# Kernel tuning notes

Hardware: AMD Instinct MI355X
Metric: run time of the kernel (lower is better)

The kernel has to match this reference:

```python
import jax, jax.numpy as jnp
import numpy as np

N = 4096
D = 256
TAU = 0.8
LAM = 0.5
K0, K1 = 64, 128


def setup_inputs() -> dict:
    key = jax.random.key(0)
    ks = jax.random.split(key, 20)
    s = 1.0 / np.sqrt(D)
    pos = (jax.random.uniform(ks[3], (N, N)) < 0.01).astype(jnp.float32)
    pos = pos.at[jnp.arange(N), jnp.arange(N)].set(1.0)  # guarantee a positive per row
    return {
        'z_mp': jax.random.normal(ks[0], (N, D), jnp.float32),
        'z_sc': jax.random.normal(ks[1], (N, D), jnp.float32),
        'feat': jax.random.normal(ks[2], (N, D), jnp.float32),
        'pos': pos,
        'im2c0': jax.random.randint(ks[4], (N,), 0, K0, jnp.int32),
        'im2c1': jax.random.randint(ks[5], (N,), 0, K1, jnp.int32),
        'centroids0': jax.random.normal(ks[6], (K0, D), jnp.float32),
        'centroids1': jax.random.normal(ks[7], (K1, D), jnp.float32),
        'density0': jax.random.uniform(ks[8], (K0,), jnp.float32) + 0.5,
        'density1': jax.random.uniform(ks[9], (K1,), jnp.float32) + 0.5,
        'pW1': jax.random.normal(ks[10], (D, D), jnp.float32) * s * 1.414,
        'pb1': jnp.zeros((D,), jnp.float32),
        'pW2': jax.random.normal(ks[11], (D, D), jnp.float32) * s * 1.414,
        'pb2': jnp.zeros((D,), jnp.float32),
        'mW1': jax.random.normal(ks[12], (D, D), jnp.float32) * s,
        'mb1': jnp.zeros((D,), jnp.float32),
        'mW2': jax.random.normal(ks[13], (D, D), jnp.float32) * s,
        'mb2': jnp.zeros((D,), jnp.float32),
    }


def _mlp(x, W1, b1, W2, b2):
    # nn.Linear -> ELU -> nn.Linear (torch Linear: x @ W.T + b)
    return jax.nn.elu(x @ W1.T + b1) @ W2.T + b2


def _sim(z1, z2, tau):
    n1 = jnp.linalg.norm(z1, axis=-1, keepdims=True)
    n2 = jnp.linalg.norm(z2, axis=-1, keepdims=True)
    return jnp.exp((z1 @ z2.T) / (n1 @ n2.T) / tau)


def _nce(sim_matrix, pos):
    m = sim_matrix / (sim_matrix.sum(axis=1, keepdims=True) + 1e-8)
    return -jnp.log((m * pos).sum(axis=-1)).mean()


def _pocl(z_anchor, z, im2cs, centroids, densities):
    n = z_anchor.shape[0]
    # weight[a,b] = #levels where a,b share a cluster (original: coo @ coo.T summed)
    sames = [(c[:, None] == c[None, :]).astype(z.dtype) for c in im2cs]
    weight = sames[0] + sames[1]
    node_prototypes = jnp.zeros_like(z)
    loss = jnp.float32(0.0)
    for same, im2c, protos, dens in zip(sames, im2cs, centroids, densities):
        # original aliases weight_clus = weight, so masking accumulates in-place
        weight = weight * same
        c = (weight @ z) / weight.sum(axis=1)[:, None]
        node_prototypes = node_prototypes + 0.1 * c
        phi = dens[im2c]
        pos_p = jnp.exp((z_anchor * node_prototypes).sum(axis=1) / phi)
        neg_p = jnp.exp((z_anchor @ protos.T) / dens).mean(axis=1) * n
        loss = loss + (-jnp.log(pos_p / neg_p)).mean()
    return loss / len(im2cs)


def reference(z_mp, z_sc, feat, pos, im2c0, im2c1, centroids0, centroids1,
              density0, density1, pW1, pb1, pW2, pb2, mW1, mb1, mW2, mb2):
    z_proj_mp = _mlp(z_mp, pW1, pb1, pW2, pb2)
    z_proj_sc = _mlp(z_sc, pW1, pb1, pW2, pb2)
    m_mp2sc = _sim(z_proj_mp, z_proj_sc, TAU)
    lori_mp = _nce(m_mp2sc, pos)
    lori_sc = _nce(m_mp2sc.T, pos)
    proto_loss = _pocl(z_sc, z_mp, [im2c0, im2c1],
                       [centroids0, centroids1], [density0, density1])
    mp_intra = _mlp(z_mp, mW1, mb1, mW2, mb2)
    loss_intramp = _nce(_sim(mp_intra, mp_intra, 0.05), pos)
    proj_mp_feat = _mlp(z_mp, pW1, pb1, pW2, pb2)
    proj_feat = _mlp(feat, pW1, pb1, pW2, pb2)
    lori_mpfeat = _nce(_sim(proj_mp_feat, proj_feat, TAU), pos)
    lori_featmp = _nce(_sim(proj_feat, proj_mp_feat, TAU), pos)
    return (LAM * lori_mp + (1 - LAM) * lori_sc + 0.3 * loss_intramp
            + proto_loss + 0.01 * lori_mpfeat + 0.01 * lori_featmp)
```

## Files before the change

kernel.cpp:

```cpp
#include <hip/hip_runtime.h>
#include <math.h>


#define NROWS 4096
#define DIM   256
#define ND    ((size_t)NROWS * DIM)

typedef unsigned short u16;
typedef unsigned int   u32;
typedef unsigned long long u64;
typedef __attribute__((ext_vector_type(8))) short bf16x8;
typedef __attribute__((ext_vector_type(4))) float f32x4;

__device__ __forceinline__ u16 f2bf(float f) {
    u32 u = __float_as_uint(f);
    return (u16)((u + 0x7fffu + ((u >> 16) & 1u)) >> 16);
}
__device__ __forceinline__ float bf2f(u16 h) {
    return __uint_as_float(((u32)h) << 16);
}

__device__ __forceinline__ void gload16(const u16* g, u16* l) {
    __builtin_amdgcn_global_load_lds(
        (const __attribute__((address_space(1))) u32*)g,
        (__attribute__((address_space(3))) u32*)l, 16, 0, 0);
}

template<int ROWS>
__device__ __forceinline__ void stage_panel(const u16* P, int kk, u16* S, int tid) {
#pragma unroll
    for (int p = 0; p < ROWS / 64; ++p) {
        const int ch = p * 256 + tid, row = ch >> 2, seg = ch & 3;
        gload16(P + (size_t)row * DIM + kk + seg * 8, &S[ch * 8]);
    }
}

__device__ __forceinline__ void wait_lgkm0() {
    asm volatile("s_waitcnt lgkmcnt(0)" ::: "memory");
    __builtin_amdgcn_sched_barrier(0);
}
template<int N> __device__ __forceinline__ void wait_vm() {
    if constexpr (N == 0)      asm volatile("s_waitcnt vmcnt(0)" ::: "memory");
    else if constexpr (N == 3) asm volatile("s_waitcnt vmcnt(3)" ::: "memory");
    else if constexpr (N == 4) asm volatile("s_waitcnt vmcnt(4)" ::: "memory");
    else if constexpr (N == 6) asm volatile("s_waitcnt vmcnt(6)" ::: "memory");
}

struct Ptr3 { const float* s0; const float* s1; const float* s2; };
__global__ __launch_bounds__(256) void cvt_in(Ptr3 p, u16* __restrict__ dst)
{
    const int z = blockIdx.y;
    const float* s = z == 0 ? p.s0 : (z == 1 ? p.s1 : p.s2);
    u16* d = dst + (size_t)z * ND;
    const int i = blockIdx.x * 256 + threadIdx.x;
    const float4 v = ((const float4*)s)[i];
    ushort4 o;
    o.x = f2bf(v.x); o.y = f2bf(v.y); o.z = f2bf(v.z); o.w = f2bf(v.w);
    ((ushort4*)d)[i] = o;
}
struct Ptr4 { const float* s0; const float* s1; const float* s2; const float* s3; };
__global__ __launch_bounds__(256) void cvt_w(Ptr4 p, u16* __restrict__ dst)
{
    const int z = blockIdx.y;
    const float* s = z == 0 ? p.s0 : (z == 1 ? p.s1 : (z == 2 ? p.s2 : p.s3));
    u16* d = dst + (size_t)z * 65536;
    const int i = blockIdx.x * 256 + threadIdx.x;
    const float4 v = ((const float4*)s)[i];
    ushort4 o;
    o.x = f2bf(v.x); o.y = f2bf(v.y); o.z = f2bf(v.z); o.w = f2bf(v.w);
    ((ushort4*)d)[i] = o;
}
__global__ __launch_bounds__(256) void cvt_cent(const float* __restrict__ c0,
                                                const float* __restrict__ c1,
                                                u16* __restrict__ CB)
{
    const int i = blockIdx.x * 256 + threadIdx.x;
    const float4 v = (i < 4096) ? ((const float4*)c0)[i]
                                : ((const float4*)c1)[i - 4096];
    ushort4 o;
    o.x = f2bf(v.x); o.y = f2bf(v.y); o.z = f2bf(v.z); o.w = f2bf(v.w);
    ((ushort4*)CB)[i] = o;
}

__global__ __launch_bounds__(256) void posbits(const float* __restrict__ pos,
                                               u64* __restrict__ bits)
{
    const int i = blockIdx.x;
    const int w = threadIdx.x >> 6, l = threadIdx.x & 63;
#pragma unroll
    for (int c = 0; c < 16; ++c) {
        const int j = c * 256 + w * 64 + l;
        const float v = pos[(size_t)i * NROWS + j];
        const u64 m = __ballot(v != 0.f);
        if (l == 0) bits[(size_t)i * 64 + c * 4 + w] = m;
    }
}

template<int ACT, int REMAP>
__global__ __launch_bounds__(256, 4) void mlp_mfma(const u16* __restrict__ IN,
                                                   const u16* __restrict__ Wp,
                                                   const u16* __restrict__ Wm,
                                                   const float* __restrict__ bp,
                                                   const float* __restrict__ bm,
                                                   u16* __restrict__ OUT)
{
    __shared__ __align__(16) u16 As[3][64 * 32];
    __shared__ __align__(16) u16 Bs[3][128 * 32];
    const int tid = threadIdx.x;
    const int bx = blockIdx.x, by = blockIdx.y;
    const bool intra = by >= 192;
    const int arow = (REMAP && intra) ? (by - 192) * 64 : by * 64;
    const u16* A = IN + (size_t)arow * DIM;
    const u16* B = (intra ? Wm : Wp) + (size_t)(bx * 128) * DIM;
    const float* bias = intra ? bm : bp;
    const int l = tid & 63, w = tid >> 6, wr = w >> 1, wc = w & 1;
    const int lr = l & 15, lk = l >> 4;

    f32x4 acc[2][4] = {};
    stage_panel<64>(A, 0, As[0], tid);
    stage_panel<128>(B, 0, Bs[0], tid);
    stage_panel<64>(A, 32, As[1], tid);
    stage_panel<128>(B, 32, Bs[1], tid);
    wait_vm<3>();
    __builtin_amdgcn_s_barrier();
#pragma unroll
    for (int t = 0; t < 8; ++t) {
        bf16x8 a[2], b[4];
#pragma unroll
        for (int mi = 0; mi < 2; ++mi)
            a[mi] = *(const bf16x8*)&As[t % 3][(wr * 32 + mi * 16 + lr) * 32 + lk * 8];
#pragma unroll
        for (int ni = 0; ni < 4; ++ni)
            b[ni] = *(const bf16x8*)&Bs[t % 3][(wc * 64 + ni * 16 + lr) * 32 + lk * 8];
        if (t < 6) {
            stage_panel<64>(A, (t + 2) * 32, As[(t + 2) % 3], tid);
            stage_panel<128>(B, (t + 2) * 32, Bs[(t + 2) % 3], tid);
        }
        wait_lgkm0();
#pragma unroll
        for (int mi = 0; mi < 2; ++mi)
#pragma unroll
            for (int ni = 0; ni < 4; ++ni)
                acc[mi][ni] = __builtin_amdgcn_mfma_f32_16x16x32_bf16(a[mi], b[ni], acc[mi][ni], 0, 0, 0);
        if (t < 6)      { wait_vm<3>(); __builtin_amdgcn_s_barrier(); }
        else if (t < 7) { wait_vm<0>(); __builtin_amdgcn_s_barrier(); }
    }

    const int j0 = bx * 128;
    float bv[4];
#pragma unroll
    for (int ni = 0; ni < 4; ++ni) bv[ni] = bias[j0 + wc * 64 + ni * 16 + lr];
#pragma unroll
    for (int mi = 0; mi < 2; ++mi)
#pragma unroll
        for (int r = 0; r < 4; ++r) {
            const int row = by * 64 + wr * 32 + mi * 16 + lk * 4 + r;
#pragma unroll
            for (int ni = 0; ni < 4; ++ni) {
                float v = acc[mi][ni][r] + bv[ni];
                if (ACT) v = v > 0.f ? v : expm1f(v);
                OUT[(size_t)row * DIM + j0 + wc * 64 + ni * 16 + lr] = f2bf(v);
            }
        }
}

__global__ __launch_bounds__(256) void rownorm_bf(u16* __restrict__ X)
{
    const int w = threadIdx.x >> 6, l = threadIdx.x & 63;
    const int row = blockIdx.x * 4 + w;
    ushort4* p = (ushort4*)(X + (size_t)row * DIM) + l;
    ushort4 u = *p;
    const float a = bf2f(u.x), b = bf2f(u.y), c = bf2f(u.z), d = bf2f(u.w);
    float ss = a * a + b * b + c * c + d * d;
#pragma unroll
    for (int m = 1; m < 64; m <<= 1) ss += __shfl_xor(ss, m);
    const float inv = rsqrtf(ss);
    u.x = f2bf(a * inv); u.y = f2bf(b * inv); u.z = f2bf(c * inv); u.w = f2bf(d * inv);
    *p = u;
}

__global__ __launch_bounds__(256, 3) void simstat3c(const u16* __restrict__ PROJ,
                                                    const u64* __restrict__ bits,
                                                    float* __restrict__ ST)
{
    const int bid = blockIdx.x;
    int z, by, bx;
    if (bid < 1024) {
        z = 0;
        const int x = bid & 7, j = bid >> 3;
        by = (x >> 1) * 8 + (j >> 4);
        bx = (x & 1) * 16 + (j & 15);
    } else if (bid < 1552) {
        z = 1;
        const int u = bid - 1024;
        const int t = (u & 7) * 66 + (u >> 3);
        int r = (int)((65.0f - sqrtf(4225.0f - 8.0f * (float)t)) * 0.5f);
        int off = 32 * r - (r * (r - 1)) / 2;
        if (t < off)                   { --r; off -= 33 - r; }
        else if (t >= off + (32 - r))  { off += 32 - r; ++r; }
        by = r; bx = r + (t - off);
    } else {
        z = 2;
        const int v = bid - 1552;
        const int x = v & 7, j = v >> 3;
        by = (x >> 1) * 8 + (j >> 4);
        bx = (x & 1) * 16 + (j & 15);
    }

    __shared__ __align__(16) u16 As[3][128 * 32];
    __shared__ __align__(16) u16 Bs[3][128 * 32];
    const int tid = threadIdx.x;
    int ao, bo;
    float* rsr; float* rsc;
    switch (z) {
        case 0:  ao = 0; bo = 1; rsr = ST + 0;     rsc = ST + 8192;  break;
        case 1:  ao = 3; bo = 3; rsr = ST + 16384; rsc = ST + 16384; break;
        default: ao = 0; bo = 2; rsr = ST + 24576; rsc = ST + 32768; break;
    }
    const float invtau = (z == 1) ? 20.f : 1.25f;
    const bool docol = (z != 1) || (bx > by);
    const int i0 = by * 128, j0 = bx * 128;
    const u16* A = PROJ + (size_t)ao * ND + (size_t)i0 * DIM;
    const u16* B = PROJ + (size_t)bo * ND + (size_t)j0 * DIM;
    const int l = tid & 63, w = tid >> 6, wr = w >> 1, wc = w & 1;
    const int lr = l & 15, lk = l >> 4;

    f32x4 acc[4][4] = {};
    stage_panel<128>(A, 0, As[0], tid);
    stage_panel<128>(B, 0, Bs[0], tid);
    stage_panel<128>(A, 32, As[1], tid);
    stage_panel<128>(B, 32, Bs[1], tid);
    wait_vm<4>();
    __builtin_amdgcn_s_barrier();
#pragma unroll
    for (int t = 0; t < 8; ++t) {
        bf16x8 a[4], b[4];
#pragma unroll
        for (int mi = 0; mi < 4; ++mi)
            a[mi] = *(const bf16x8*)&As[t % 3][(wr * 64 + mi * 16 + lr) * 32 + lk * 8];
#pragma unroll
        for (int ni = 0; ni < 4; ++ni)
            b[ni] = *(const bf16x8*)&Bs[t % 3][(wc * 64 + ni * 16 + lr) * 32 + lk * 8];
        if (t < 6) {
            stage_panel<128>(A, (t + 2) * 32, As[(t + 2) % 3], tid);
            stage_panel<128>(B, (t + 2) * 32, Bs[(t + 2) % 3], tid);
        }
        wait_lgkm0();
#pragma unroll
        for (int mi = 0; mi < 4; ++mi)
#pragma unroll
            for (int ni = 0; ni < 4; ++ni)
                acc[mi][ni] = __builtin_amdgcn_mfma_f32_16x16x32_bf16(a[mi], b[ni], acc[mi][ni], 0, 0, 0);
        if (t < 6)      { wait_vm<4>(); __builtin_amdgcn_s_barrier(); }
        else if (t < 7) { wait_vm<0>(); __builtin_amdgcn_s_barrier(); }
    }

#pragma unroll
    for (int mi = 0; mi < 4; ++mi)
#pragma unroll
        for (int ni = 0; ni < 4; ++ni)
#pragma unroll
            for (int r = 0; r < 4; ++r)
                acc[mi][ni][r] = __expf(acc[mi][ni][r] * invtau);

#pragma unroll
    for (int mi = 0; mi < 4; ++mi)
#pragma unroll
        for (int r = 0; r < 4; ++r) {
            const int i = i0 + wr * 64 + mi * 16 + lk * 4 + r;
            const u64 pw = bits[(size_t)i * 64 + bx * 2 + wc];
            float rsum = 0.f, psum = 0.f;
#pragma unroll
            for (int ni = 0; ni < 4; ++ni) {
                const float ev = acc[mi][ni][r];
                rsum += ev;
                psum += ((pw >> (ni * 16 + lr)) & 1ull) ? ev : 0.f;
            }
#pragma unroll
            for (int m = 1; m < 16; m <<= 1) {
                rsum += __shfl_xor(rsum, m);
                psum += __shfl_xor(psum, m);
            }
            if (lr == 0) {
                atomicAdd(&rsr[i], rsum);
                atomicAdd(&rsr[4096 + i], psum);
            }
        }

    if (docol) {
#pragma unroll
        for (int ni = 0; ni < 4; ++ni) {
            const int j = j0 + wc * 64 + ni * 16 + lr;
            const u64 pw = bits[(size_t)j * 64 + by * 2 + wr];
            float csum = 0.f, qsum = 0.f;
#pragma unroll
            for (int mi = 0; mi < 4; ++mi)
#pragma unroll
                for (int r = 0; r < 4; ++r) {
                    const float ev = acc[mi][ni][r];
                    csum += ev;
                    qsum += ((pw >> (mi * 16 + lk * 4 + r)) & 1ull) ? ev : 0.f;
                }
            csum += __shfl_xor(csum, 16); csum += __shfl_xor(csum, 32);
            qsum += __shfl_xor(qsum, 16); qsum += __shfl_xor(qsum, 32);
            if (lk == 0) {
                atomicAdd(&rsc[j], csum);
                atomicAdd(&rsc[4096 + j], qsum);
            }
        }
    }
}

__global__ __launch_bounds__(256, 4) void gcent_mfma(const u16* __restrict__ Zb,
                                                     const u16* __restrict__ CB,
                                                     float* __restrict__ G)
{
    __shared__ __align__(16) u16 As[3][128 * 32];
    __shared__ __align__(16) u16 Bs[3][64 * 32];
    const int tid = threadIdx.x;
    const int bx = blockIdx.x, by = blockIdx.y;
    const int i0 = by * 128, j0 = bx * 64;
    const u16* A = Zb + (size_t)i0 * DIM;
    const u16* B = CB + (size_t)j0 * DIM;
    const int l = tid & 63, w = tid >> 6, wr = w >> 1, wc = w & 1;
    const int lr = l & 15, lk = l >> 4;

    f32x4 acc[4][2] = {};
    stage_panel<128>(A, 0, As[0], tid);
    stage_panel<64>(B, 0, Bs[0], tid);
    stage_panel<128>(A, 32, As[1], tid);
    stage_panel<64>(B, 32, Bs[1], tid);
    wait_vm<3>();
    __builtin_amdgcn_s_barrier();
#pragma unroll
    for (int t = 0; t < 8; ++t) {
        bf16x8 a[4], b[2];
#pragma unroll
        for (int mi = 0; mi < 4; ++mi)
            a[mi] = *(const bf16x8*)&As[t % 3][(wr * 64 + mi * 16 + lr) * 32 + lk * 8];
#pragma unroll
        for (int ni = 0; ni < 2; ++ni)
            b[ni] = *(const bf16x8*)&Bs[t % 3][(wc * 32 + ni * 16 + lr) * 32 + lk * 8];
        if (t < 6) {
            stage_panel<128>(A, (t + 2) * 32, As[(t + 2) % 3], tid);
            stage_panel<64>(B, (t + 2) * 32, Bs[(t + 2) % 3], tid);
        }
        wait_lgkm0();
#pragma unroll
        for (int mi = 0; mi < 4; ++mi)
#pragma unroll
            for (int ni = 0; ni < 2; ++ni)
                acc[mi][ni] = __builtin_amdgcn_mfma_f32_16x16x32_bf16(a[mi], b[ni], acc[mi][ni], 0, 0, 0);
        if (t < 6)      { wait_vm<3>(); __builtin_amdgcn_s_barrier(); }
        else if (t < 7) { wait_vm<0>(); __builtin_amdgcn_s_barrier(); }
    }

#pragma unroll
    for (int mi = 0; mi < 4; ++mi)
#pragma unroll
        for (int r = 0; r < 4; ++r) {
            const int row = i0 + wr * 64 + mi * 16 + lk * 4 + r;
#pragma unroll
            for (int ni = 0; ni < 2; ++ni)
                G[(size_t)row * 192 + j0 + wc * 32 + ni * 16 + lr] = acc[mi][ni][r];
        }
}

__global__ __launch_bounds__(256) void scatter_pairs(const float* __restrict__ z,
                                                     const int* __restrict__ i0a,
                                                     const int* __restrict__ i1a,
                                                     float* __restrict__ S01,
                                                     float* __restrict__ cnt01)
{
    const int b = blockIdx.x, d = threadIdx.x;
    const int p = i0a[b] * 128 + i1a[b];
    atomicAdd(&S01[(size_t)p * DIM + d], z[(size_t)b * DIM + d]);
    if (d == 0) atomicAdd(&cnt01[p], 1.f);
}

__global__ __launch_bounds__(256) void reduce_pairs(const float* __restrict__ S01,
                                                    const float* __restrict__ cnt01,
                                                    float* __restrict__ S0,
                                                    float* __restrict__ cnt0)
{
    const int k0 = blockIdx.x, d = threadIdx.x;
    float s = 0.f;
    for (int k1 = 0; k1 < 128; ++k1)
        s += S01[(size_t)(k0 * 128 + k1) * DIM + d];
    S0[(size_t)k0 * DIM + d] = s;
    __shared__ float c[128];
    if (d < 128) c[d] = cnt01[k0 * 128 + d];
    __syncthreads();
    if (d == 0) {
        float t = 0.f;
        for (int i = 0; i < 128; ++i) t += c[i];
        cnt0[k0] = t;
    }
}

__global__ __launch_bounds__(256) void pocl_row(const float* __restrict__ z_sc,
                                                const int* __restrict__ i0a,
                                                const int* __restrict__ i1a,
                                                const float* __restrict__ S0,
                                                const float* __restrict__ S01,
                                                const float* __restrict__ cnt0,
                                                const float* __restrict__ cnt01,
                                                const float* __restrict__ G,
                                                const float* __restrict__ d0,
                                                const float* __restrict__ d1,
                                                float* __restrict__ L1,
                                                float* __restrict__ L2)
{
    const int w = threadIdx.x >> 6, l = threadIdx.x & 63;
    const int a = blockIdx.x * 4 + w;
    const int k0 = i0a[a], k1 = i1a[a];
    const int p = k0 * 128 + k1;
    const float n0 = cnt0[k0], n01 = cnt01[p];
    const float inv1 = 1.f / (n0 + n01), inv2 = 1.f / n01;
    const float4 s0  = *(const float4*)&S0[(size_t)k0 * DIM + l * 4];
    const float4 s01 = *(const float4*)&S01[(size_t)p * DIM + l * 4];
    const float4 zd  = *(const float4*)&z_sc[(size_t)a * DIM + l * 4];

    float dot1 = 0.f, dot2 = 0.f;
    {
        const float c1x = (s0.x + s01.x) * inv1, c2x = s01.x * inv2;
        const float c1y = (s0.y + s01.y) * inv1, c2y = s01.y * inv2;
        const float c1z = (s0.z + s01.z) * inv1, c2z = s01.z * inv2;
        const float c1w = (s0.w + s01.w) * inv1, c2w = s01.w * inv2;
        dot1 = zd.x * c1x + zd.y * c1y + zd.z * c1z + zd.w * c1w;
        dot2 = zd.x * (c1x + c2x) + zd.y * (c1y + c2y) + zd.z * (c1z + c2z) + zd.w * (c1w + c2w);
    }
    dot1 *= 0.1f; dot2 *= 0.1f;
#pragma unroll
    for (int m = 1; m < 64; m <<= 1) {
        dot1 += __shfl_xor(dot1, m);
        dot2 += __shfl_xor(dot2, m);
    }

    const float x0 = G[(size_t)a * 192 + l] / d0[l];
    float M0 = x0;
#pragma unroll
    for (int m = 1; m < 64; m <<= 1) M0 = fmaxf(M0, __shfl_xor(M0, m));
    float e0 = __expf(x0 - M0);
#pragma unroll
    for (int m = 1; m < 64; m <<= 1) e0 += __shfl_xor(e0, m);

    const float x1a = G[(size_t)a * 192 + 64 + l] / d1[l];
    const float x1b = G[(size_t)a * 192 + 128 + l] / d1[64 + l];
    float M1 = fmaxf(x1a, x1b);
#pragma unroll
    for (int m = 1; m < 64; m <<= 1) M1 = fmaxf(M1, __shfl_xor(M1, m));
    float e1 = __expf(x1a - M1) + __expf(x1b - M1);
#pragma unroll
    for (int m = 1; m < 64; m <<= 1) e1 += __shfl_xor(e1, m);

    if (l == 0) {
        const float lneg1 = M0 + logf(e0) - logf(64.f)  + logf(4096.f);
        const float lneg2 = M1 + logf(e1) - logf(128.f) + logf(4096.f);
        L1[a] = lneg1 - dot1 / d0[k0];
        L2[a] = lneg2 - dot2 / d1[k1];
    }
}

__global__ __launch_bounds__(256) void final_reduce(const float* __restrict__ st,
                                                    const float* __restrict__ L1,
                                                    const float* __restrict__ L2,
                                                    float* __restrict__ out)
{
    const int t = threadIdx.x;
    const float* rs0 = st + 0;      const float* pr0 = st + 4096;
    const float* rs1 = st + 8192;   const float* pr1 = st + 12288;
    const float* rs2 = st + 16384;  const float* pr2 = st + 20480;
    const float* rs3 = st + 24576;  const float* pr3 = st + 28672;
    const float* rs4 = st + 32768;  const float* pr4 = st + 36864;

    float acc = 0.f;
    for (int i = t; i < NROWS; i += 256) {
        const float lmp = logf(rs0[i] + 1e-8f) - logf(pr0[i]);
        const float lsc = logf(rs1[i] + 1e-8f) - logf(pr1[i]);
        const float lin = logf(rs2[i] + 1e-8f) - logf(pr2[i]);
        const float lmf = logf(rs3[i] + 1e-8f) - logf(pr3[i]);
        const float lfm = logf(rs4[i] + 1e-8f) - logf(pr4[i]);
        acc += 0.5f * (lmp + lsc) + 0.3f * lin
             + 0.01f * (lmf + lfm) + 0.5f * (L1[i] + L2[i]);
    }
    __shared__ float red[256];
    red[t] = acc; __syncthreads();
    for (int s = 128; s > 0; s >>= 1) {
        if (t < s) red[t] += red[t + s];
        __syncthreads();
    }
    if (t == 0) out[0] = red[0] * (1.f / 4096.f);
}

extern "C" void kernel_launch(void* const* d_in, const int* in_sizes, int n_in,
                              void* d_out, int out_size, void* d_ws, size_t ws_size,
                              hipStream_t stream)
{
    const float* z_mp = (const float*)d_in[0];
    const float* z_sc = (const float*)d_in[1];
    const float* feat = (const float*)d_in[2];
    const float* pos  = (const float*)d_in[3];
    const int*   im0  = (const int*)d_in[4];
    const int*   im1  = (const int*)d_in[5];
    const float* c0   = (const float*)d_in[6];
    const float* c1   = (const float*)d_in[7];
    const float* d0   = (const float*)d_in[8];
    const float* d1   = (const float*)d_in[9];
    const float* pW1  = (const float*)d_in[10];
    const float* pb1  = (const float*)d_in[11];
    const float* pW2  = (const float*)d_in[12];
    const float* pb2  = (const float*)d_in[13];
    const float* mW1  = (const float*)d_in[14];
    const float* mb1  = (const float*)d_in[15];
    const float* mW2  = (const float*)d_in[16];
    const float* mb2  = (const float*)d_in[17];
    float* out = (float*)d_out;
    float* ws  = (float*)d_ws;
    (void)in_sizes; (void)n_in; (void)out_size; (void)ws_size;

    float* ST   = ws;
    float* S0f  = ST + 40960;
    float* CN0  = S0f + 16384;
    float* CN01 = CN0 + 64;
    float* S01f = CN01 + 8192;
    float* ZEND = S01f + (size_t)8192 * DIM;
    float* G    = ZEND;
    float* L1   = G + (size_t)NROWS * 192;
    float* L2   = L1 + NROWS;
    u64*  bits  = (u64*)(L2 + NROWS);
    u16*  INb   = (u16*)(bits + (size_t)NROWS * 64);
    u16*  Hb    = INb + 3 * ND;
    u16*  PROJ  = Hb + 4 * ND;
    u16*  Wb    = PROJ + 4 * ND;
    u16*  CB    = Wb + 4 * 65536;

    hipMemsetAsync(ws, 0, (size_t)(ZEND - ws) * sizeof(float), stream);

    const dim3 blk(256);

    Ptr3 pin{z_mp, z_sc, feat};
    cvt_in<<<dim3(1024, 3), blk, 0, stream>>>(pin, INb);
    Ptr4 pw{pW1, pW2, mW1, mW2};
    cvt_w<<<dim3(64, 4), blk, 0, stream>>>(pw, Wb);
    cvt_cent<<<48, blk, 0, stream>>>(c0, c1, CB);

    posbits<<<NROWS, blk, 0, stream>>>(pos, bits);

    mlp_mfma<1, 1><<<dim3(2, 256), blk, 0, stream>>>(INb, Wb, Wb + 2 * 65536,
                                                     pb1, mb1, Hb);
    mlp_mfma<0, 0><<<dim3(2, 256), blk, 0, stream>>>(Hb, Wb + 65536, Wb + 3 * 65536,
                                                     pb2, mb2, PROJ);
    rownorm_bf<<<4096, blk, 0, stream>>>(PROJ);

    simstat3c<<<2576, blk, 0, stream>>>(PROJ, bits, ST);

    scatter_pairs<<<NROWS, blk, 0, stream>>>(z_mp, im0, im1, S01f, CN01);
    reduce_pairs<<<64, blk, 0, stream>>>(S01f, CN01, S0f, CN0);
    gcent_mfma<<<dim3(3, 32), blk, 0, stream>>>(INb + ND, CB, G);
    pocl_row<<<1024, blk, 0, stream>>>(z_sc, im0, im1, S0f, S01f, CN0, CN01,
                                       G, d0, d1, L1, L2);

    final_reduce<<<1, blk, 0, stream>>>(ST, L1, L2, out);
}
```

Before: 163.9 us.

## Shrink GEMM tiles to double-buffered 64-wide tiles and drop symmetric-tile skipping

```diff
diff --git a/kernel.cpp b/kernel.cpp
--- a/kernel.cpp
+++ b/kernel.cpp
@@ -41,9 +41,8 @@
 }
 template<int N> __device__ __forceinline__ void wait_vm() {
     if constexpr (N == 0)      asm volatile("s_waitcnt vmcnt(0)" ::: "memory");
+    else if constexpr (N == 2) asm volatile("s_waitcnt vmcnt(2)" ::: "memory");
     else if constexpr (N == 3) asm volatile("s_waitcnt vmcnt(3)" ::: "memory");
-    else if constexpr (N == 4) asm volatile("s_waitcnt vmcnt(4)" ::: "memory");
-    else if constexpr (N == 6) asm volatile("s_waitcnt vmcnt(6)" ::: "memory");
 }
 
 struct Ptr3 { const float* s0; const float* s1; const float* s2; };
@@ -104,15 +103,107 @@
                                                    const float* __restrict__ bm,
                                                    u16* __restrict__ OUT)
 {
-    __shared__ __align__(16) u16 As[3][64 * 32];
-    __shared__ __align__(16) u16 Bs[3][128 * 32];
+    __shared__ __align__(16) u16 As[2][64 * 32];
+    __shared__ __align__(16) u16 Bs[2][64 * 32];
     const int tid = threadIdx.x;
     const int bx = blockIdx.x, by = blockIdx.y;
     const bool intra = by >= 192;
     const int arow = (REMAP && intra) ? (by - 192) * 64 : by * 64;
     const u16* A = IN + (size_t)arow * DIM;
-    const u16* B = (intra ? Wm : Wp) + (size_t)(bx * 128) * DIM;
+    const u16* B = (intra ? Wm : Wp) + (size_t)(bx * 64) * DIM;
     const float* bias = intra ? bm : bp;
+    const int l = tid & 63, w = tid >> 6, wr = w >> 1, wc = w & 1;
+    const int lr = l & 15, lk = l >> 4;
+
+    f32x4 acc[2][2] = {};
+    stage_panel<64>(A, 0, As[0], tid);
+    stage_panel<64>(B, 0, Bs[0], tid);
+    stage_panel<64>(A, 32, As[1], tid);
+    stage_panel<64>(B, 32, Bs[1], tid);
+    wait_vm<2>();
+    __builtin_amdgcn_s_barrier();
+#pragma unroll
+    for (int t = 0; t < 8; ++t) {
+        bf16x8 a[2], b[2];
+#pragma unroll
+        for (int mi = 0; mi < 2; ++mi)
+            a[mi] = *(const bf16x8*)&As[t & 1][(wr * 32 + mi * 16 + lr) * 32 + lk * 8];
+#pragma unroll
+        for (int ni = 0; ni < 2; ++ni)
+            b[ni] = *(const bf16x8*)&Bs[t & 1][(wc * 32 + ni * 16 + lr) * 32 + lk * 8];
+        wait_lgkm0();
+        __builtin_amdgcn_s_barrier();
+        if (t < 6) {
+            stage_panel<64>(A, (t + 2) * 32, As[t & 1], tid);
+            stage_panel<64>(B, (t + 2) * 32, Bs[t & 1], tid);
+        }
+#pragma unroll
+        for (int mi = 0; mi < 2; ++mi)
+#pragma unroll
+            for (int ni = 0; ni < 2; ++ni)
+                acc[mi][ni] = __builtin_amdgcn_mfma_f32_16x16x32_bf16(a[mi], b[ni], acc[mi][ni], 0, 0, 0);
+        if (t < 6)      { wait_vm<2>(); __builtin_amdgcn_s_barrier(); }
+        else if (t < 7) { wait_vm<0>(); __builtin_amdgcn_s_barrier(); }
+    }
+
+    const int j0 = bx * 64;
+    float bv[2];
+#pragma unroll
+    for (int ni = 0; ni < 2; ++ni) bv[ni] = bias[j0 + wc * 32 + ni * 16 + lr];
+#pragma unroll
+    for (int mi = 0; mi < 2; ++mi)
+#pragma unroll
+        for (int r = 0; r < 4; ++r) {
+            const int row = by * 64 + wr * 32 + mi * 16 + lk * 4 + r;
+#pragma unroll
+            for (int ni = 0; ni < 2; ++ni) {
+                float v = acc[mi][ni][r] + bv[ni];
+                if (ACT) v = v > 0.f ? v : expm1f(v);
+                OUT[(size_t)row * DIM + j0 + wc * 32 + ni * 16 + lr] = f2bf(v);
+            }
+        }
+}
+
+__global__ __launch_bounds__(256) void rownorm_bf(u16* __restrict__ X)
+{
+    const int w = threadIdx.x >> 6, l = threadIdx.x & 63;
+    const int row = blockIdx.x * 4 + w;
+    ushort4* p = (ushort4*)(X + (size_t)row * DIM) + l;
+    ushort4 u = *p;
+    const float a = bf2f(u.x), b = bf2f(u.y), c = bf2f(u.z), d = bf2f(u.w);
+    float ss = a * a + b * b + c * c + d * d;
+#pragma unroll
+    for (int m = 1; m < 64; m <<= 1) ss += __shfl_xor(ss, m);
+    const float inv = rsqrtf(ss);
+    u.x = f2bf(a * inv); u.y = f2bf(b * inv); u.z = f2bf(c * inv); u.w = f2bf(d * inv);
+    *p = u;
+}
+
+__global__ __launch_bounds__(256, 5) void simstat3c(const u16* __restrict__ PROJ,
+                                                    const u64* __restrict__ bits,
+                                                    float* __restrict__ ST)
+{
+    const int bid = blockIdx.x;
+    const int z = bid >> 11;
+    const int q = bid & 2047;
+    const int by = q >> 5;
+    const int bx = q & 31;
+
+    __shared__ __align__(16) u16 As[2][64 * 32];
+    __shared__ __align__(16) u16 Bs[2][128 * 32];
+    const int tid = threadIdx.x;
+    int ao, bo;
+    float* rsr; float* rsc;
+    switch (z) {
+        case 0:  ao = 0; bo = 1; rsr = ST + 0;     rsc = ST + 8192;  break;
+        case 1:  ao = 3; bo = 3; rsr = ST + 16384; rsc = ST + 16384; break;
+        default: ao = 0; bo = 2; rsr = ST + 24576; rsc = ST + 32768; break;
+    }
+    const float invtau = (z == 1) ? 20.f : 1.25f;
+    const bool docol = (z != 1);
+    const int i0 = by * 64, j0 = bx * 128;
+    const u16* A = PROJ + (size_t)ao * ND + (size_t)i0 * DIM;
+    const u16* B = PROJ + (size_t)bo * ND + (size_t)j0 * DIM;
     const int l = tid & 63, w = tid >> 6, wr = w >> 1, wc = w & 1;
     const int lr = l & 15, lk = l >> 4;
 
@@ -128,15 +219,16 @@
         bf16x8 a[2], b[4];
 #pragma unroll
         for (int mi = 0; mi < 2; ++mi)
-            a[mi] = *(const bf16x8*)&As[t % 3][(wr * 32 + mi * 16 + lr) * 32 + lk * 8];
+            a[mi] = *(const bf16x8*)&As[t & 1][(wr * 32 + mi * 16 + lr) * 32 + lk * 8];
 #pragma unroll
         for (int ni = 0; ni < 4; ++ni)
-            b[ni] = *(const bf16x8*)&Bs[t % 3][(wc * 64 + ni * 16 + lr) * 32 + lk * 8];
+            b[ni] = *(const bf16x8*)&Bs[t & 1][(wc * 64 + ni * 16 + lr) * 32 + lk * 8];
+        wait_lgkm0();
+        __builtin_amdgcn_s_barrier();
         if (t < 6) {
-            stage_panel<64>(A, (t + 2) * 32, As[(t + 2) % 3], tid);
-            stage_panel<128>(B, (t + 2) * 32, Bs[(t + 2) % 3], tid);
-        }
-        wait_lgkm0();
+            stage_panel<64>(A, (t + 2) * 32, As[t & 1], tid);
+            stage_panel<128>(B, (t + 2) * 32, Bs[t & 1], tid);
+        }
 #pragma unroll
         for (int mi = 0; mi < 2; ++mi)
 #pragma unroll
@@ -146,117 +238,8 @@
         else if (t < 7) { wait_vm<0>(); __builtin_amdgcn_s_barrier(); }
     }
 
-    const int j0 = bx * 128;
-    float bv[4];
-#pragma unroll
-    for (int ni = 0; ni < 4; ++ni) bv[ni] = bias[j0 + wc * 64 + ni * 16 + lr];
 #pragma unroll
     for (int mi = 0; mi < 2; ++mi)
-#pragma unroll
-        for (int r = 0; r < 4; ++r) {
-            const int row = by * 64 + wr * 32 + mi * 16 + lk * 4 + r;
-#pragma unroll
-            for (int ni = 0; ni < 4; ++ni) {
-                float v = acc[mi][ni][r] + bv[ni];
-                if (ACT) v = v > 0.f ? v : expm1f(v);
-                OUT[(size_t)row * DIM + j0 + wc * 64 + ni * 16 + lr] = f2bf(v);
-            }
-        }
-}
-
-__global__ __launch_bounds__(256) void rownorm_bf(u16* __restrict__ X)
-{
-    const int w = threadIdx.x >> 6, l = threadIdx.x & 63;
-    const int row = blockIdx.x * 4 + w;
-    ushort4* p = (ushort4*)(X + (size_t)row * DIM) + l;
-    ushort4 u = *p;
-    const float a = bf2f(u.x), b = bf2f(u.y), c = bf2f(u.z), d = bf2f(u.w);
-    float ss = a * a + b * b + c * c + d * d;
-#pragma unroll
-    for (int m = 1; m < 64; m <<= 1) ss += __shfl_xor(ss, m);
-    const float inv = rsqrtf(ss);
-    u.x = f2bf(a * inv); u.y = f2bf(b * inv); u.z = f2bf(c * inv); u.w = f2bf(d * inv);
-    *p = u;
-}
-
-__global__ __launch_bounds__(256, 3) void simstat3c(const u16* __restrict__ PROJ,
-                                                    const u64* __restrict__ bits,
-                                                    float* __restrict__ ST)
-{
-    const int bid = blockIdx.x;
-    int z, by, bx;
-    if (bid < 1024) {
-        z = 0;
-        const int x = bid & 7, j = bid >> 3;
-        by = (x >> 1) * 8 + (j >> 4);
-        bx = (x & 1) * 16 + (j & 15);
-    } else if (bid < 1552) {
-        z = 1;
-        const int u = bid - 1024;
-        const int t = (u & 7) * 66 + (u >> 3);
-        int r = (int)((65.0f - sqrtf(4225.0f - 8.0f * (float)t)) * 0.5f);
-        int off = 32 * r - (r * (r - 1)) / 2;
-        if (t < off)                   { --r; off -= 33 - r; }
-        else if (t >= off + (32 - r))  { off += 32 - r; ++r; }
-        by = r; bx = r + (t - off);
-    } else {
-        z = 2;
-        const int v = bid - 1552;
-        const int x = v & 7, j = v >> 3;
-        by = (x >> 1) * 8 + (j >> 4);
-        bx = (x & 1) * 16 + (j & 15);
-    }
-
-    __shared__ __align__(16) u16 As[3][128 * 32];
-    __shared__ __align__(16) u16 Bs[3][128 * 32];
-    const int tid = threadIdx.x;
-    int ao, bo;
-    float* rsr; float* rsc;
-    switch (z) {
-        case 0:  ao = 0; bo = 1; rsr = ST + 0;     rsc = ST + 8192;  break;
-        case 1:  ao = 3; bo = 3; rsr = ST + 16384; rsc = ST + 16384; break;
-        default: ao = 0; bo = 2; rsr = ST + 24576; rsc = ST + 32768; break;
-    }
-    const float invtau = (z == 1) ? 20.f : 1.25f;
-    const bool docol = (z != 1) || (bx > by);
-    const int i0 = by * 128, j0 = bx * 128;
-    const u16* A = PROJ + (size_t)ao * ND + (size_t)i0 * DIM;
-    const u16* B = PROJ + (size_t)bo * ND + (size_t)j0 * DIM;
-    const int l = tid & 63, w = tid >> 6, wr = w >> 1, wc = w & 1;
-    const int lr = l & 15, lk = l >> 4;
-
-    f32x4 acc[4][4] = {};
-    stage_panel<128>(A, 0, As[0], tid);
-    stage_panel<128>(B, 0, Bs[0], tid);
-    stage_panel<128>(A, 32, As[1], tid);
-    stage_panel<128>(B, 32, Bs[1], tid);
-    wait_vm<4>();
-    __builtin_amdgcn_s_barrier();
-#pragma unroll
-    for (int t = 0; t < 8; ++t) {
-        bf16x8 a[4], b[4];
-#pragma unroll
-        for (int mi = 0; mi < 4; ++mi)
-            a[mi] = *(const bf16x8*)&As[t % 3][(wr * 64 + mi * 16 + lr) * 32 + lk * 8];
-#pragma unroll
-        for (int ni = 0; ni < 4; ++ni)
-            b[ni] = *(const bf16x8*)&Bs[t % 3][(wc * 64 + ni * 16 + lr) * 32 + lk * 8];
-        if (t < 6) {
-            stage_panel<128>(A, (t + 2) * 32, As[(t + 2) % 3], tid);
-            stage_panel<128>(B, (t + 2) * 32, Bs[(t + 2) % 3], tid);
-        }
-        wait_lgkm0();
-#pragma unroll
-        for (int mi = 0; mi < 4; ++mi)
-#pragma unroll
-            for (int ni = 0; ni < 4; ++ni)
-                acc[mi][ni] = __builtin_amdgcn_mfma_f32_16x16x32_bf16(a[mi], b[ni], acc[mi][ni], 0, 0, 0);
-        if (t < 6)      { wait_vm<4>(); __builtin_amdgcn_s_barrier(); }
-        else if (t < 7) { wait_vm<0>(); __builtin_amdgcn_s_barrier(); }
-    }
-
-#pragma unroll
-    for (int mi = 0; mi < 4; ++mi)
 #pragma unroll
         for (int ni = 0; ni < 4; ++ni)
 #pragma unroll
@@ -264,10 +247,10 @@
                 acc[mi][ni][r] = __expf(acc[mi][ni][r] * invtau);
 
 #pragma unroll
-    for (int mi = 0; mi < 4; ++mi)
+    for (int mi = 0; mi < 2; ++mi)
 #pragma unroll
         for (int r = 0; r < 4; ++r) {
-            const int i = i0 + wr * 64 + mi * 16 + lk * 4 + r;
+            const int i = i0 + wr * 32 + mi * 16 + lk * 4 + r;
             const u64 pw = bits[(size_t)i * 64 + bx * 2 + wc];
             float rsum = 0.f, psum = 0.f;
 #pragma unroll
@@ -291,15 +274,15 @@
 #pragma unroll
         for (int ni = 0; ni < 4; ++ni) {
             const int j = j0 + wc * 64 + ni * 16 + lr;
-            const u64 pw = bits[(size_t)j * 64 + by * 2 + wr];
+            const u64 pw = bits[(size_t)j * 64 + by];
             float csum = 0.f, qsum = 0.f;
 #pragma unroll
-            for (int mi = 0; mi < 4; ++mi)
+            for (int mi = 0; mi < 2; ++mi)
 #pragma unroll
                 for (int r = 0; r < 4; ++r) {
                     const float ev = acc[mi][ni][r];
                     csum += ev;
-                    qsum += ((pw >> (mi * 16 + lk * 4 + r)) & 1ull) ? ev : 0.f;
+                    qsum += ((pw >> (wr * 32 + mi * 16 + lk * 4 + r)) & 1ull) ? ev : 0.f;
                 }
             csum += __shfl_xor(csum, 16); csum += __shfl_xor(csum, 32);
             qsum += __shfl_xor(qsum, 16); qsum += __shfl_xor(qsum, 32);
@@ -547,13 +530,13 @@
 
     posbits<<<NROWS, blk, 0, stream>>>(pos, bits);
 
-    mlp_mfma<1, 1><<<dim3(2, 256), blk, 0, stream>>>(INb, Wb, Wb + 2 * 65536,
+    mlp_mfma<1, 1><<<dim3(4, 256), blk, 0, stream>>>(INb, Wb, Wb + 2 * 65536,
                                                      pb1, mb1, Hb);
-    mlp_mfma<0, 0><<<dim3(2, 256), blk, 0, stream>>>(Hb, Wb + 65536, Wb + 3 * 65536,
+    mlp_mfma<0, 0><<<dim3(4, 256), blk, 0, stream>>>(Hb, Wb + 65536, Wb + 3 * 65536,
                                                      pb2, mb2, PROJ);
     rownorm_bf<<<4096, blk, 0, stream>>>(PROJ);
 
-    simstat3c<<<2576, blk, 0, stream>>>(PROJ, bits, ST);
+    simstat3c<<<6144, blk, 0, stream>>>(PROJ, bits, ST);
 
     scatter_pairs<<<NROWS, blk, 0, stream>>>(z_mp, im0, im1, S01f, CN01);
     reduce_pairs<<<64, blk, 0, stream>>>(S01f, CN01, S0f, CN0);
```

After: 175.2 us. +6.9%, slower.

## Restructure similarity-stat GEMM into barrier-free per-wave tiles with swizzled LDS

Applied to the files above, without the earlier changes.

```diff
diff --git a/kernel.cpp b/kernel.cpp
--- a/kernel.cpp
+++ b/kernel.cpp
@@ -35,6 +35,16 @@
     }
 }
 
+template<int ROWS>
+__device__ __forceinline__ void stage_wave(const u16* P, int kk, u16* dst, int l) {
+#pragma unroll
+    for (int p = 0; p < ROWS / 16; ++p) {
+        const int ch = p * 64 + l, row = ch >> 2, seg = ch & 3;
+        const int sseg = seg ^ ((row >> 1) & 3);
+        gload16(P + (size_t)row * DIM + kk + sseg * 8, dst + ch * 8);
+    }
+}
+
 __device__ __forceinline__ void wait_lgkm0() {
     asm volatile("s_waitcnt lgkmcnt(0)" ::: "memory");
     __builtin_amdgcn_sched_barrier(0);
@@ -42,7 +52,6 @@
 template<int N> __device__ __forceinline__ void wait_vm() {
     if constexpr (N == 0)      asm volatile("s_waitcnt vmcnt(0)" ::: "memory");
     else if constexpr (N == 3) asm volatile("s_waitcnt vmcnt(3)" ::: "memory");
-    else if constexpr (N == 4) asm volatile("s_waitcnt vmcnt(4)" ::: "memory");
     else if constexpr (N == 6) asm volatile("s_waitcnt vmcnt(6)" ::: "memory");
 }
 
@@ -179,37 +188,22 @@
     *p = u;
 }
 
-__global__ __launch_bounds__(256, 3) void simstat3c(const u16* __restrict__ PROJ,
+__global__ __launch_bounds__(256, 3) void simstat3w(const u16* __restrict__ PROJ,
                                                     const u64* __restrict__ bits,
                                                     float* __restrict__ ST)
 {
+    __shared__ __align__(16) u16 SB[4][6144];
+    const int tid = threadIdx.x;
+    const int w = tid >> 6, l = tid & 63;
+    const int lr = l & 15, lk = l >> 4;
+
     const int bid = blockIdx.x;
-    int z, by, bx;
-    if (bid < 1024) {
-        z = 0;
-        const int x = bid & 7, j = bid >> 3;
-        by = (x >> 1) * 8 + (j >> 4);
-        bx = (x & 1) * 16 + (j & 15);
-    } else if (bid < 1552) {
-        z = 1;
-        const int u = bid - 1024;
-        const int t = (u & 7) * 66 + (u >> 3);
-        int r = (int)((65.0f - sqrtf(4225.0f - 8.0f * (float)t)) * 0.5f);
-        int off = 32 * r - (r * (r - 1)) / 2;
-        if (t < off)                   { --r; off -= 33 - r; }
-        else if (t >= off + (32 - r))  { off += 32 - r; ++r; }
-        by = r; bx = r + (t - off);
-    } else {
-        z = 2;
-        const int v = bid - 1552;
-        const int x = v & 7, j = v >> 3;
-        by = (x >> 1) * 8 + (j >> 4);
-        bx = (x & 1) * 16 + (j & 15);
-    }
-
-    __shared__ __align__(16) u16 As[3][128 * 32];
-    __shared__ __align__(16) u16 Bs[3][128 * 32];
-    const int tid = threadIdx.x;
+    const int z = bid >> 11;
+    const int q = bid & 2047;
+    const int it = q >> 4;
+    const int jt = ((q & 15) << 2) + w;
+    const int i0 = it * 32, j0 = jt * 64;
+
     int ao, bo;
     float* rsr; float* rsc;
     switch (z) {
@@ -218,45 +212,47 @@
         default: ao = 0; bo = 2; rsr = ST + 24576; rsc = ST + 32768; break;
     }
     const float invtau = (z == 1) ? 20.f : 1.25f;
-    const bool docol = (z != 1) || (bx > by);
-    const int i0 = by * 128, j0 = bx * 128;
     const u16* A = PROJ + (size_t)ao * ND + (size_t)i0 * DIM;
     const u16* B = PROJ + (size_t)bo * ND + (size_t)j0 * DIM;
-    const int l = tid & 63, w = tid >> 6, wr = w >> 1, wc = w & 1;
-    const int lr = l & 15, lk = l >> 4;
-
-    f32x4 acc[4][4] = {};
-    stage_panel<128>(A, 0, As[0], tid);
-    stage_panel<128>(B, 0, Bs[0], tid);
-    stage_panel<128>(A, 32, As[1], tid);
-    stage_panel<128>(B, 32, Bs[1], tid);
-    wait_vm<4>();
-    __builtin_amdgcn_s_barrier();
+
+    u16* A0 = SB[w];
+    u16* A1 = SB[w] + 1024;
+    u16* B0 = SB[w] + 2048;
+    u16* B1 = SB[w] + 4096;
+
+    f32x4 acc[2][4] = {};
+    stage_wave<32>(A, 0, A0, l);
+    stage_wave<64>(B, 0, B0, l);
+    stage_wave<32>(A, 32, A1, l);
+    stage_wave<64>(B, 32, B1, l);
+
+    const int xo = (lr >> 1) & 3;
 #pragma unroll
     for (int t = 0; t < 8; ++t) {
-        bf16x8 a[4], b[4];
-#pragma unroll
-        for (int mi = 0; mi < 4; ++mi)
-            a[mi] = *(const bf16x8*)&As[t % 3][(wr * 64 + mi * 16 + lr) * 32 + lk * 8];
+        u16* Ab = (t & 1) ? A1 : A0;
+        u16* Bb = (t & 1) ? B1 : B0;
+        if (t == 7) wait_vm<0>(); else wait_vm<6>();
+        bf16x8 a[2], b[4];
+#pragma unroll
+        for (int mi = 0; mi < 2; ++mi)
+            a[mi] = *(const bf16x8*)&Ab[(mi * 16 + lr) * 32 + (lk ^ xo) * 8];
 #pragma unroll
         for (int ni = 0; ni < 4; ++ni)
-            b[ni] = *(const bf16x8*)&Bs[t % 3][(wc * 64 + ni * 16 + lr) * 32 + lk * 8];
+            b[ni] = *(const bf16x8*)&Bb[(ni * 16 + lr) * 32 + (lk ^ xo) * 8];
+        wait_lgkm0();
         if (t < 6) {
-            stage_panel<128>(A, (t + 2) * 32, As[(t + 2) % 3], tid);
-            stage_panel<128>(B, (t + 2) * 32, Bs[(t + 2) % 3], tid);
-        }
-        wait_lgkm0();
-#pragma unroll
-        for (int mi = 0; mi < 4; ++mi)
+            stage_wave<32>(A, (t + 2) * 32, Ab, l);
+            stage_wave<64>(B, (t + 2) * 32, Bb, l);
+        }
+#pragma unroll
+        for (int mi = 0; mi < 2; ++mi)
 #pragma unroll
             for (int ni = 0; ni < 4; ++ni)
                 acc[mi][ni] = __builtin_amdgcn_mfma_f32_16x16x32_bf16(a[mi], b[ni], acc[mi][ni], 0, 0, 0);
-        if (t < 6)      { wait_vm<4>(); __builtin_amdgcn_s_barrier(); }
-        else if (t < 7) { wait_vm<0>(); __builtin_amdgcn_s_barrier(); }
-    }
-
-#pragma unroll
-    for (int mi = 0; mi < 4; ++mi)
+    }
+
+#pragma unroll
+    for (int mi = 0; mi < 2; ++mi)
 #pragma unroll
         for (int ni = 0; ni < 4; ++ni)
 #pragma unroll
@@ -264,11 +260,11 @@
                 acc[mi][ni][r] = __expf(acc[mi][ni][r] * invtau);
 
 #pragma unroll
-    for (int mi = 0; mi < 4; ++mi)
+    for (int mi = 0; mi < 2; ++mi)
 #pragma unroll
         for (int r = 0; r < 4; ++r) {
-            const int i = i0 + wr * 64 + mi * 16 + lk * 4 + r;
-            const u64 pw = bits[(size_t)i * 64 + bx * 2 + wc];
+            const int i = i0 + mi * 16 + lk * 4 + r;
+            const u64 pw = bits[(size_t)i * 64 + jt];
             float rsum = 0.f, psum = 0.f;
 #pragma unroll
             for (int ni = 0; ni < 4; ++ni) {
@@ -287,19 +283,20 @@
             }
         }
 
-    if (docol) {
+    if (z != 1) {
+        const int ib = i0 >> 6, sh = i0 & 32;
 #pragma unroll
         for (int ni = 0; ni < 4; ++ni) {
-            const int j = j0 + wc * 64 + ni * 16 + lr;
-            const u64 pw = bits[(size_t)j * 64 + by * 2 + wr];
+            const int j = j0 + ni * 16 + lr;
+            const u64 pw = bits[(size_t)j * 64 + ib];
             float csum = 0.f, qsum = 0.f;
 #pragma unroll
-            for (int mi = 0; mi < 4; ++mi)
+            for (int mi = 0; mi < 2; ++mi)
 #pragma unroll
                 for (int r = 0; r < 4; ++r) {
                     const float ev = acc[mi][ni][r];
                     csum += ev;
-                    qsum += ((pw >> (mi * 16 + lk * 4 + r)) & 1ull) ? ev : 0.f;
+                    qsum += ((pw >> (sh + mi * 16 + lk * 4 + r)) & 1ull) ? ev : 0.f;
                 }
             csum += __shfl_xor(csum, 16); csum += __shfl_xor(csum, 32);
             qsum += __shfl_xor(qsum, 16); qsum += __shfl_xor(qsum, 32);
@@ -553,7 +550,7 @@
                                                      pb2, mb2, PROJ);
     rownorm_bf<<<4096, blk, 0, stream>>>(PROJ);
 
-    simstat3c<<<2576, blk, 0, stream>>>(PROJ, bits, ST);
+    simstat3w<<<6144, blk, 0, stream>>>(PROJ, bits, ST);
 
     scatter_pairs<<<NROWS, blk, 0, stream>>>(z_mp, im0, im1, S01f, CN01);
     reduce_pairs<<<64, blk, 0, stream>>>(S01f, CN01, S0f, CN0);
```

Result: slower. 203.7 us (+24.3%).

## Load simstat MFMA operands directly from global and merge conversion kernels

Applied to the files above, without the earlier changes.

```diff
diff --git a/kernel.cpp b/kernel.cpp
--- a/kernel.cpp
+++ b/kernel.cpp
@@ -42,44 +42,45 @@
 template<int N> __device__ __forceinline__ void wait_vm() {
     if constexpr (N == 0)      asm volatile("s_waitcnt vmcnt(0)" ::: "memory");
     else if constexpr (N == 3) asm volatile("s_waitcnt vmcnt(3)" ::: "memory");
-    else if constexpr (N == 4) asm volatile("s_waitcnt vmcnt(4)" ::: "memory");
-    else if constexpr (N == 6) asm volatile("s_waitcnt vmcnt(6)" ::: "memory");
-}
-
-struct Ptr3 { const float* s0; const float* s1; const float* s2; };
-__global__ __launch_bounds__(256) void cvt_in(Ptr3 p, u16* __restrict__ dst)
+}
+
+struct PtrAll {
+    const float* in0; const float* in1; const float* in2;
+    const float* w0; const float* w1; const float* w2; const float* w3;
+    const float* c0; const float* c1;
+};
+__global__ __launch_bounds__(256) void cvt_all(PtrAll p, u16* __restrict__ INb,
+                                               u16* __restrict__ Wb,
+                                               u16* __restrict__ CB)
 {
     const int z = blockIdx.y;
-    const float* s = z == 0 ? p.s0 : (z == 1 ? p.s1 : p.s2);
-    u16* d = dst + (size_t)z * ND;
-    const int i = blockIdx.x * 256 + threadIdx.x;
-    const float4 v = ((const float4*)s)[i];
-    ushort4 o;
-    o.x = f2bf(v.x); o.y = f2bf(v.y); o.z = f2bf(v.z); o.w = f2bf(v.w);
-    ((ushort4*)d)[i] = o;
-}
-struct Ptr4 { const float* s0; const float* s1; const float* s2; const float* s3; };
-__global__ __launch_bounds__(256) void cvt_w(Ptr4 p, u16* __restrict__ dst)
-{
-    const int z = blockIdx.y;
-    const float* s = z == 0 ? p.s0 : (z == 1 ? p.s1 : (z == 2 ? p.s2 : p.s3));
-    u16* d = dst + (size_t)z * 65536;
-    const int i = blockIdx.x * 256 + threadIdx.x;
-    const float4 v = ((const float4*)s)[i];
-    ushort4 o;
-    o.x = f2bf(v.x); o.y = f2bf(v.y); o.z = f2bf(v.z); o.w = f2bf(v.w);
-    ((ushort4*)d)[i] = o;
-}
-__global__ __launch_bounds__(256) void cvt_cent(const float* __restrict__ c0,
-                                                const float* __restrict__ c1,
-                                                u16* __restrict__ CB)
-{
-    const int i = blockIdx.x * 256 + threadIdx.x;
-    const float4 v = (i < 4096) ? ((const float4*)c0)[i]
-                                : ((const float4*)c1)[i - 4096];
-    ushort4 o;
-    o.x = f2bf(v.x); o.y = f2bf(v.y); o.z = f2bf(v.z); o.w = f2bf(v.w);
-    ((ushort4*)CB)[i] = o;
+    if (z < 3) {
+        const float* s = z == 0 ? p.in0 : (z == 1 ? p.in1 : p.in2);
+        u16* d = INb + (size_t)z * ND;
+        const int i = blockIdx.x * 256 + threadIdx.x;
+        const float4 v = ((const float4*)s)[i];
+        ushort4 o;
+        o.x = f2bf(v.x); o.y = f2bf(v.y); o.z = f2bf(v.z); o.w = f2bf(v.w);
+        ((ushort4*)d)[i] = o;
+    } else {
+        const int b = blockIdx.x;
+        if (b < 256) {
+            const int wi = b >> 6;
+            const float* s = wi == 0 ? p.w0 : (wi == 1 ? p.w1 : (wi == 2 ? p.w2 : p.w3));
+            const int i = (b & 63) * 256 + threadIdx.x;
+            const float4 v = ((const float4*)s)[i];
+            ushort4 o;
+            o.x = f2bf(v.x); o.y = f2bf(v.y); o.z = f2bf(v.z); o.w = f2bf(v.w);
+            ((ushort4*)(Wb + (size_t)wi * 65536))[i] = o;
+        } else if (b < 304) {
+            const int i = (b - 256) * 256 + threadIdx.x;
+            const float4 v = (i < 4096) ? ((const float4*)p.c0)[i]
+                                        : ((const float4*)p.c1)[i - 4096];
+            ushort4 o;
+            o.x = f2bf(v.x); o.y = f2bf(v.y); o.z = f2bf(v.z); o.w = f2bf(v.w);
+            ((ushort4*)CB)[i] = o;
+        }
+    }
 }
 
 __global__ __launch_bounds__(256) void posbits(const float* __restrict__ pos,
@@ -179,37 +180,20 @@
     *p = u;
 }
 
-__global__ __launch_bounds__(256, 3) void simstat3c(const u16* __restrict__ PROJ,
+__global__ __launch_bounds__(256, 3) void simstat3r(const u16* __restrict__ PROJ,
                                                     const u64* __restrict__ bits,
                                                     float* __restrict__ ST)
 {
+    const int tid = threadIdx.x;
+    const int w = tid >> 6, l = tid & 63;
+    const int lr = l & 15, lk = l >> 4;
+    const int wr = w >> 1, wc = w & 1;
+
     const int bid = blockIdx.x;
-    int z, by, bx;
-    if (bid < 1024) {
-        z = 0;
-        const int x = bid & 7, j = bid >> 3;
-        by = (x >> 1) * 8 + (j >> 4);
-        bx = (x & 1) * 16 + (j & 15);
-    } else if (bid < 1552) {
-        z = 1;
-        const int u = bid - 1024;
-        const int t = (u & 7) * 66 + (u >> 3);
-        int r = (int)((65.0f - sqrtf(4225.0f - 8.0f * (float)t)) * 0.5f);
-        int off = 32 * r - (r * (r - 1)) / 2;
-        if (t < off)                   { --r; off -= 33 - r; }
-        else if (t >= off + (32 - r))  { off += 32 - r; ++r; }
-        by = r; bx = r + (t - off);
-    } else {
-        z = 2;
-        const int v = bid - 1552;
-        const int x = v & 7, j = v >> 3;
-        by = (x >> 1) * 8 + (j >> 4);
-        bx = (x & 1) * 16 + (j & 15);
-    }
-
-    __shared__ __align__(16) u16 As[3][128 * 32];
-    __shared__ __align__(16) u16 Bs[3][128 * 32];
-    const int tid = threadIdx.x;
+    const int z = bid >> 10;
+    const int q = bid & 1023;
+    const int by = q >> 5, bx = q & 31;
+
     int ao, bo;
     float* rsr; float* rsc;
     switch (z) {
@@ -218,41 +202,26 @@
         default: ao = 0; bo = 2; rsr = ST + 24576; rsc = ST + 32768; break;
     }
     const float invtau = (z == 1) ? 20.f : 1.25f;
-    const bool docol = (z != 1) || (bx > by);
     const int i0 = by * 128, j0 = bx * 128;
-    const u16* A = PROJ + (size_t)ao * ND + (size_t)i0 * DIM;
-    const u16* B = PROJ + (size_t)bo * ND + (size_t)j0 * DIM;
-    const int l = tid & 63, w = tid >> 6, wr = w >> 1, wc = w & 1;
-    const int lr = l & 15, lk = l >> 4;
+
+    const u16* ap = PROJ + (size_t)ao * ND + (size_t)(i0 + wr * 64 + lr) * DIM + lk * 8;
+    const u16* bp = PROJ + (size_t)bo * ND + (size_t)(j0 + wc * 64 + lr) * DIM + lk * 8;
 
     f32x4 acc[4][4] = {};
-    stage_panel<128>(A, 0, As[0], tid);
-    stage_panel<128>(B, 0, Bs[0], tid);
-    stage_panel<128>(A, 32, As[1], tid);
-    stage_panel<128>(B, 32, Bs[1], tid);
-    wait_vm<4>();
-    __builtin_amdgcn_s_barrier();
 #pragma unroll
     for (int t = 0; t < 8; ++t) {
         bf16x8 a[4], b[4];
 #pragma unroll
         for (int mi = 0; mi < 4; ++mi)
-            a[mi] = *(const bf16x8*)&As[t % 3][(wr * 64 + mi * 16 + lr) * 32 + lk * 8];
+            a[mi] = *(const bf16x8*)(ap + (size_t)mi * 16 * DIM + t * 32);
 #pragma unroll
         for (int ni = 0; ni < 4; ++ni)
-            b[ni] = *(const bf16x8*)&Bs[t % 3][(wc * 64 + ni * 16 + lr) * 32 + lk * 8];
-        if (t < 6) {
-            stage_panel<128>(A, (t + 2) * 32, As[(t + 2) % 3], tid);
-            stage_panel<128>(B, (t + 2) * 32, Bs[(t + 2) % 3], tid);
-        }
-        wait_lgkm0();
+            b[ni] = *(const bf16x8*)(bp + (size_t)ni * 16 * DIM + t * 32);
 #pragma unroll
         for (int mi = 0; mi < 4; ++mi)
 #pragma unroll
             for (int ni = 0; ni < 4; ++ni)
                 acc[mi][ni] = __builtin_amdgcn_mfma_f32_16x16x32_bf16(a[mi], b[ni], acc[mi][ni], 0, 0, 0);
-        if (t < 6)      { wait_vm<4>(); __builtin_amdgcn_s_barrier(); }
-        else if (t < 7) { wait_vm<0>(); __builtin_amdgcn_s_barrier(); }
     }
 
 #pragma unroll
@@ -287,7 +256,7 @@
             }
         }
 
-    if (docol) {
+    if (z != 1) {
 #pragma unroll
         for (int ni = 0; ni < 4; ++ni) {
             const int j = j0 + wc * 64 + ni * 16 + lr;
@@ -539,11 +508,8 @@
 
     const dim3 blk(256);
 
-    Ptr3 pin{z_mp, z_sc, feat};
-    cvt_in<<<dim3(1024, 3), blk, 0, stream>>>(pin, INb);
-    Ptr4 pw{pW1, pW2, mW1, mW2};
-    cvt_w<<<dim3(64, 4), blk, 0, stream>>>(pw, Wb);
-    cvt_cent<<<48, blk, 0, stream>>>(c0, c1, CB);
+    PtrAll pall{z_mp, z_sc, feat, pW1, pW2, mW1, mW2, c0, c1};
+    cvt_all<<<dim3(1024, 4), blk, 0, stream>>>(pall, INb, Wb, CB);
 
     posbits<<<NROWS, blk, 0, stream>>>(pos, bits);
 
@@ -553,7 +519,7 @@
                                                      pb2, mb2, PROJ);
     rownorm_bf<<<4096, blk, 0, stream>>>(PROJ);
 
-    simstat3c<<<2576, blk, 0, stream>>>(PROJ, bits, ST);
+    simstat3r<<<3072, blk, 0, stream>>>(PROJ, bits, ST);
 
     scatter_pairs<<<NROWS, blk, 0, stream>>>(z_mp, im0, im1, S01f, CN01);
     reduce_pairs<<<64, blk, 0, stream>>>(S01f, CN01, S0f, CN0);
```

Result: slower. 197.0 us (+20.2%).
